# Optimization experiments

Hardware: AMD Instinct MI355X
Metric: run time of the kernel (lower is better)

The kernel has to match this reference:

```python
import jax, jax.numpy as jnp
import numpy as np

N = 10000      # nodes
E = 320000     # edges
H = 128        # hidden_features
GF = 12        # graph-level features
L = 6          # gnn layers
EPS = 1e-5


def _glorot(key, shape):
    fan_in = shape[0]
    return (jax.random.normal(key, shape, jnp.float32) / np.sqrt(fan_in)).astype(jnp.float32)


def periodic_difference(x_i, x_j, domain):
    diff = x_i - x_j
    # (1 - 2*(x_i < x_j)) * domain  ==  +domain if x_i >= x_j else -domain
    shift = jnp.where(x_i < x_j, -domain, domain)
    diff_shifted = diff - shift
    return jnp.where(jnp.abs(diff) < jnp.abs(diff_shifted), diff, diff_shifted)


def _mlp2_relu(x, W1, b1, W2, b2):
    # Linear -> ReLU -> Linear -> ReLU
    return jax.nn.relu(jax.nn.relu(x @ W1 + b1) @ W2 + b2)


def setup_inputs() -> dict:
    key = jax.random.key(0)
    ks = jax.random.split(key, 32)
    inp = {
        "v": jax.random.normal(ks[0], (N, 6), jnp.float32),
        "pos": jax.random.uniform(ks[1], (N, 3), jnp.float32),
        "r": jax.random.uniform(ks[2], (N, 1), jnp.float32),
        "domain": jnp.ones((3,), jnp.float32),
        "t": jax.random.uniform(ks[3], (1,), jnp.float32),
        "x_global": jax.random.normal(ks[4], (4,), jnp.float32),
        "domain_next": jnp.ones((3,), jnp.float32),
        "t_next": jax.random.uniform(ks[5], (1,), jnp.float32),
        "edge_index": jax.random.randint(ks[6], (2, E), 0, N, jnp.int32),
        "batch": jnp.zeros((N,), jnp.int32),
    }
    # embedding MLP: 19 -> H -> H
    inp["emb_W1"] = _glorot(ks[7], (19, H)); inp["emb_b1"] = jnp.zeros((H,), jnp.float32)
    inp["emb_W2"] = _glorot(ks[8], (H, H)); inp["emb_b2"] = jnp.zeros((H,), jnp.float32)
    # per-layer message net: 157 -> H -> H ; update net: 268 -> H -> H
    msg_in = H + GF + 3 + 2 * (6 + 1)   # 157
    upd_in = H + H + GF                 # 268
    inp["msg_W1"] = jnp.stack([_glorot(jax.random.fold_in(ks[9], i), (msg_in, H)) for i in range(L)])
    inp["msg_b1"] = jnp.zeros((L, H), jnp.float32)
    inp["msg_W2"] = jnp.stack([_glorot(jax.random.fold_in(ks[10], i), (H, H)) for i in range(L)])
    inp["msg_b2"] = jnp.zeros((L, H), jnp.float32)
    inp["upd_W1"] = jnp.stack([_glorot(jax.random.fold_in(ks[11], i), (upd_in, H)) for i in range(L)])
    inp["upd_b1"] = jnp.zeros((L, H), jnp.float32)
    inp["upd_W2"] = jnp.stack([_glorot(jax.random.fold_in(ks[12], i), (H, H)) for i in range(L)])
    inp["upd_b2"] = jnp.zeros((L, H), jnp.float32)
    # output MLP: H -> H -> 9 ; macro MLP: H -> H -> 3
    inp["out_W1"] = _glorot(ks[13], (H, H)); inp["out_b1"] = jnp.zeros((H,), jnp.float32)
    inp["out_W2"] = _glorot(ks[14], (H, 9)); inp["out_b2"] = jnp.zeros((9,), jnp.float32)
    inp["mac_W1"] = _glorot(ks[15], (H, H)); inp["mac_b1"] = jnp.zeros((H,), jnp.float32)
    inp["mac_W2"] = _glorot(ks[16], (H, 3)); inp["mac_b2"] = jnp.zeros((3,), jnp.float32)
    return inp


def reference(v, pos, r, domain, t, x_global, domain_next, t_next, edge_index, batch,
              emb_W1, emb_b1, emb_W2, emb_b2,
              msg_W1, msg_b1, msg_W2, msg_b2,
              upd_W1, upd_b1, upd_W2, upd_b2,
              out_W1, out_b1, out_W2, out_b2,
              mac_W1, mac_b1, mac_W2, mac_b2):
    n = v.shape[0]
    gf = jnp.concatenate([domain, t, x_global, domain_next, t_next])          # [12]
    gf_n = jnp.broadcast_to(gf, (n, GF))
    node_features = jnp.concatenate([pos, v], axis=1)                         # [N, 9]

    # embedding (positions excluded)
    h = _mlp2_relu(jnp.concatenate([r, v, gf_n], axis=1), emb_W1, emb_b1, emb_W2, emb_b2)

    src, dst = edge_index[0], edge_index[1]   # j = source, i = target (PyG default)
    gf_e = jnp.broadcast_to(gf, (src.shape[0], GF))
    counts = jax.ops.segment_sum(jnp.ones(src.shape, h.dtype), dst, num_segments=N)
    inv_counts = (1.0 / jnp.maximum(counts, 1.0))[:, None]

    pos_diff = periodic_difference(pos[dst], pos[src], domain)                # [E, 3]
    v_i, v_j, r_i, r_j = v[dst], v[src], r[dst], r[src]

    for l in range(L):
        h_i, h_j = h[dst], h[src]
        msg_in = jnp.concatenate([h_i - h_j, v_i, v_j, r_i, r_j, pos_diff, gf_e], axis=1)
        m = _mlp2_relu(msg_in, msg_W1[l], msg_b1[l], msg_W2[l], msg_b2[l])    # [E, H]
        agg = jax.ops.segment_sum(m, dst, num_segments=N) * inv_counts        # scatter-mean
        upd_in = jnp.concatenate([h, agg, gf_n], axis=1)
        u = _mlp2_relu(upd_in, upd_W1[l], upd_b1[l], upd_W2[l], upd_b2[l])
        h = u + h                                                              # residual (in==out)
        # InstanceNorm over each graph (single graph here), biased variance
        mu = h.mean(axis=0, keepdims=True)
        var = h.var(axis=0, keepdims=True)
        h = (h - mu) / jnp.sqrt(var + EPS)

    prediction = jax.nn.relu(h @ out_W1 + out_b1) @ out_W2 + out_b2 + node_features
    pred_x = jnp.remainder(prediction[:, :3], domain_next)
    pred_v = prediction[:, 3:]
    h_mean = h.mean(axis=0)                                                    # global mean pool, 1 graph
    pred_macro = jax.nn.relu(h_mean @ mac_W1 + mac_b1) @ mac_W2 + mac_b2
    return pred_x, pred_v, pred_macro
```

## Files before the change

### kernel.cpp

```cpp
#include <hip/hip_runtime.h>
#include <hip/hip_bf16.h>

#define NN 10000
#define NE 320000
#define HD 128
#define NL 6
#define EPSV 1e-5f

typedef _Float16 half8  __attribute__((ext_vector_type(8)));
typedef _Float16 half4v __attribute__((ext_vector_type(4)));
typedef float    f32x4  __attribute__((ext_vector_type(4)));

__device__ __forceinline__ float relu_(float x){ return fmaxf(x, 0.0f); }


__global__ void k_degree(const int* __restrict__ dst, int* __restrict__ counts){
  int e = blockIdx.x*256 + threadIdx.x;
  if (e < NE) atomicAdd(&counts[dst[e]], 1);
}

__global__ void k_scan(const int* __restrict__ counts, int* __restrict__ offs, float* __restrict__ invc){
  __shared__ int lds[1024];
  __shared__ int base_s;
  int tid = threadIdx.x;
  if (tid==0) base_s = 0;
  __syncthreads();
  for (int start=0; start<NN; start+=1024){
    int i = start+tid;
    int vv = (i<NN)? counts[i] : 0;
    lds[tid]=vv; __syncthreads();
    for (int off=1; off<1024; off<<=1){
      int t = (tid>=off)? lds[tid-off] : 0;
      __syncthreads();
      lds[tid] += t;
      __syncthreads();
    }
    int incl = lds[tid];
    if (i<NN){
      offs[i] = base_s + incl - vv;
      invc[i] = 1.0f / fmaxf((float)vv, 1.0f);
    }
    __syncthreads();
    if (tid==1023) base_s += lds[1023];
    __syncthreads();
  }
  if (tid==0) offs[NN] = base_s;
}

__global__ void k_place(const int* __restrict__ src, const int* __restrict__ dst,
                        const int* __restrict__ offs, int* __restrict__ cursor, int* __restrict__ csr){
  int e = blockIdx.x*256 + threadIdx.x;
  if (e < NE){
    int d = dst[e];
    int p = atomicAdd(&cursor[d], 1);
    csr[offs[d]+p] = src[e];
  }
}


__global__ void k_biasfold(const float* __restrict__ dom, const float* __restrict__ tt,
                           const float* __restrict__ xg, const float* __restrict__ domn,
                           const float* __restrict__ tn,
                           const float* __restrict__ embW1, const float* __restrict__ embB1,
                           const float* __restrict__ msgW1, const float* __restrict__ msgB1,
                           const float* __restrict__ updW1, const float* __restrict__ updB1,
                           float* __restrict__ b1eff, float* __restrict__ mu, float* __restrict__ rstd){
  float gf[12];
  gf[0]=dom[0]; gf[1]=dom[1]; gf[2]=dom[2]; gf[3]=tt[0];
  gf[4]=xg[0]; gf[5]=xg[1]; gf[6]=xg[2]; gf[7]=xg[3];
  gf[8]=domn[0]; gf[9]=domn[1]; gf[10]=domn[2]; gf[11]=tn[0];
  int b = blockIdx.x, t = threadIdx.x;
  if (b==0){
    float s = embB1[t];
    #pragma unroll
    for (int k=0;k<12;++k) s += gf[k]*embW1[(7+k)*HD + t];
    b1eff[t] = s;
  } else if (b<=6){
    int l=b-1;
    float s = msgB1[l*HD+t];
    #pragma unroll
    for (int k=0;k<12;++k) s += gf[k]*msgW1[((size_t)l*157 + 145+k)*HD + t];
    b1eff[(1+l)*HD + t] = s;
  } else if (b<=12){
    int l=b-7;
    float s = updB1[l*HD+t];
    #pragma unroll
    for (int k=0;k<12;++k) s += gf[k]*updW1[((size_t)l*268 + 256+k)*HD + t];
    b1eff[(7+l)*HD + t] = s;
  } else {
    mu[t] = 0.f;
    rstd[t] = 1.f;
  }
}


__global__ __launch_bounds__(512,1) void k_embed(
    const float* __restrict__ r, const float* __restrict__ v,
    const float* __restrict__ W1, const float* __restrict__ b1e,
    const float* __restrict__ W2, const float* __restrict__ b2,
    float* __restrict__ hb){
  __shared__ alignas(16) _Float16 Ahi[16*136];
  __shared__ alignas(16) _Float16 Alo[16*136];
  int tid = threadIdx.x;
  int n0 = blockIdx.x*16;
  if (tid < 256){
    int node = tid>>4, chunk = tid&15;
    int n = n0 + node;
    int f = chunk*8;
    float in7[7];
    in7[0]=r[n];
    #pragma unroll
    for (int k=0;k<6;++k) in7[1+k]=v[n*6+k];
    half8 ah, al;
    #pragma unroll
    for (int j=0;j<8;++j){
      float z = b1e[f+j];
      #pragma unroll
      for (int k=0;k<7;++k) z += in7[k]*W1[k*HD + f+j];
      float a = fmaxf(z, 0.f);
      _Float16 h = (_Float16)a;
      ah[j] = h; al[j] = (_Float16)(a - (float)h);
    }
    *(half8*)&Ahi[node*136 + f] = ah;
    *(half8*)&Alo[node*136 + f] = al;
  }
  int wid = tid>>6, lane = tid&63, g = lane>>4, c = lane&15;
  int col = 16*wid + c;
  half8 bh[4], bl[4];
  #pragma unroll
  for (int ks=0; ks<4; ++ks){
    half8 fh, fl;
    #pragma unroll
    for (int j=0;j<8;++j){
      float w = W2[(size_t)(ks*32 + g*8 + j)*HD + col];
      _Float16 h = (_Float16)w;
      fh[j]=h; fl[j]=(_Float16)(w - (float)h);
    }
    bh[ks]=fh; bl[ks]=fl;
  }
  float b2c = b2[col];
  f32x4 zero4 = {0.f,0.f,0.f,0.f};
  __syncthreads();
  f32x4 d = zero4;
  #pragma unroll
  for (int ks=0; ks<4; ++ks){
    half8 ah = *(const half8*)&Ahi[c*136 + ks*32 + g*8];
    half8 al = *(const half8*)&Alo[c*136 + ks*32 + g*8];
    d = __builtin_amdgcn_mfma_f32_16x16x32_f16(ah, bh[ks], d, 0,0,0);
    d = __builtin_amdgcn_mfma_f32_16x16x32_f16(al, bh[ks], d, 0,0,0);
    d = __builtin_amdgcn_mfma_f32_16x16x32_f16(ah, bl[ks], d, 0,0,0);
  }
  #pragma unroll
  for (int jj=0;jj<4;++jj){
    int n = n0 + g*4 + jj;
    hb[(size_t)n*HD + col] = fmaxf(d[jj] + b2c, 0.f);
  }
}


__global__ __launch_bounds__(512,1) void k_hW(
    const float* __restrict__ hb, const float* __restrict__ mu, const float* __restrict__ rstd,
    const float* __restrict__ v, const float* __restrict__ r,
    const float* __restrict__ W, const float* __restrict__ b1e,
    float* __restrict__ P, float* __restrict__ Q){
  __shared__ alignas(16) _Float16 Xhi[16*136];
  __shared__ alignas(16) _Float16 Xlo[16*136];
  int tid = threadIdx.x;
  int n0 = blockIdx.x*16;
  if (tid < 256){
    int node = tid>>4, chunk = tid&15;
    int n = n0 + node;
    int f = chunk*8;
    half8 xh, xl;
    #pragma unroll
    for (int j=0;j<8;++j){
      float x = (hb[(size_t)n*HD + f+j] - mu[f+j]) * rstd[f+j];
      _Float16 h = (_Float16)x;
      xh[j] = h; xl[j] = (_Float16)(x - (float)h);
    }
    *(half8*)&Xhi[node*136 + f] = xh;
    *(half8*)&Xlo[node*136 + f] = xl;
  }
  int wid = tid>>6, lane = tid&63, g = lane>>4, c = lane&15;
  int col = 16*wid + c;
  half8 bh[4], bl[4];
  #pragma unroll
  for (int ks=0; ks<4; ++ks){
    half8 fh, fl;
    #pragma unroll
    for (int j=0;j<8;++j){
      float w = W[(size_t)(ks*32 + g*8 + j)*HD + col];
      _Float16 h = (_Float16)w;
      fh[j]=h; fl[j]=(_Float16)(w - (float)h);
    }
    bh[ks]=fh; bl[ks]=fl;
  }
  float wvi[6], wvj[6];
  #pragma unroll
  for (int x=0;x<6;++x){
    wvi[x]=W[(size_t)(128+x)*HD+col];
    wvj[x]=W[(size_t)(134+x)*HD+col];
  }
  float wri=W[(size_t)140*HD+col], wrj=W[(size_t)141*HD+col];
  float b1c=b1e[col];
  f32x4 zero4 = {0.f,0.f,0.f,0.f};
  __syncthreads();
  f32x4 d = zero4;
  #pragma unroll
  for (int ks=0; ks<4; ++ks){
    half8 ah = *(const half8*)&Xhi[c*136 + ks*32 + g*8];
    half8 al = *(const half8*)&Xlo[c*136 + ks*32 + g*8];
    d = __builtin_amdgcn_mfma_f32_16x16x32_f16(ah, bh[ks], d, 0,0,0);
    d = __builtin_amdgcn_mfma_f32_16x16x32_f16(al, bh[ks], d, 0,0,0);
    d = __builtin_amdgcn_mfma_f32_16x16x32_f16(ah, bl[ks], d, 0,0,0);
  }
  #pragma unroll
  for (int jj=0;jj<4;++jj){
    int n = n0 + g*4 + jj;
    float m = d[jj];
    float p = m + b1c, q = -m;
    #pragma unroll
    for (int x=0;x<6;++x){
      float vx = v[n*6+x];
      p += vx*wvi[x]; q += vx*wvj[x];
    }
    float rn = r[n];
    p += rn*wri; q += rn*wrj;
    P[(size_t)n*HD+col]=p;
    Q[(size_t)n*HD+col]=q;
  }
}


__global__ __launch_bounds__(256,2) void k_edge(
    const float* __restrict__ P, const float* __restrict__ Q,
    const float* __restrict__ pos, const float* __restrict__ dom,
    const int* __restrict__ offs, const int* __restrict__ csr,
    const float* __restrict__ Wpd, const float* __restrict__ W2, const float* __restrict__ b2,
    const float* __restrict__ invc, float* __restrict__ agg,
    float* __restrict__ zsum, float* __restrict__ zsumsq){
  __shared__ alignas(16) _Float16 w1pd[128*40];
  __shared__ alignas(16) _Float16 a1hi[16*136];
  __shared__ alignas(16) _Float16 a1lo[16*136];
  int tid = threadIdx.x;
  if (blockIdx.x==0 && tid<HD){ zsum[tid]=0.f; zsumsq[tid]=0.f; }
  if (tid < 128){
    int f = tid;
    #pragma unroll
    for (int k=0;k<32;++k) w1pd[f*40+k] = (_Float16)0.f;
    #pragma unroll
    for (int x=0;x<3;++x){
      float w = Wpd[x*HD + f];
      _Float16 h = (_Float16)w;
      w1pd[f*40 + x]     = h;
      w1pd[f*40 + 3 + x] = h;
      w1pd[f*40 + 6 + x] = (_Float16)(w - (float)h);
    }
  }
  int wid = tid>>6, lane = tid&63, g = lane>>4, c = lane&15;
  int t0 = 2*wid, t1 = 2*wid+1;
  half8 w2h[4][2], w2l[4][2];
  #pragma unroll
  for (int ks=0; ks<4; ++ks){
    #pragma unroll
    for (int tt=0; tt<2; ++tt){
      int col = 16*(2*wid+tt) + c;
      half8 fh, fl;
      #pragma unroll
      for (int j=0;j<8;++j){
        float w = W2[(ks*32 + g*8 + j)*HD + col];
        _Float16 h = (_Float16)w;
        fh[j] = h;
        fl[j] = (_Float16)(w - (float)h);
      }
      w2h[ks][tt] = fh;
      w2l[ks][tt] = fl;
    }
  }
  float b2v0 = b2[16*t0 + c], b2v1 = b2[16*t1 + c];
  float dm0=dom[0], dm1=dom[1], dm2=dom[2];
  f32x4 zero4 = {0.f,0.f,0.f,0.f};
  __syncthreads();
  int n0 = blockIdx.x*2;
  for (int n = n0; n < n0+2; ++n){
    f32x4 pv0 = *(const f32x4*)(P + (size_t)n*HD + 16*t0 + 4*g);
    f32x4 pv1 = *(const f32x4*)(P + (size_t)n*HD + 16*t1 + 4*g);
    float pn0=pos[n*3+0], pn1=pos[n*3+1], pn2=pos[n*3+2];
    float acc0=0.f, acc1=0.f;
    int ib=offs[n], ie=offs[n+1];
    for (int base=ib; base<ie; base+=16){
      int nb = ie - base; if (nb>16) nb = 16;
      int sA = csr[base + ((c<nb)? c : nb-1)];
      float q0=pos[sA*3+0], q1=pos[sA*3+1], q2=pos[sA*3+2];
      float pd0,pd1,pd2;
      { float diff,sh,ds;
        diff=pn0-q0; sh=(pn0<q0)?-dm0:dm0; ds=diff-sh; pd0=(fabsf(diff)<fabsf(ds))?diff:ds;
        diff=pn1-q1; sh=(pn1<q1)?-dm1:dm1; ds=diff-sh; pd1=(fabsf(diff)<fabsf(ds))?diff:ds;
        diff=pn2-q2; sh=(pn2<q2)?-dm2:dm2; ds=diff-sh; pd2=(fabsf(diff)<fabsf(ds))?diff:ds;
      }
      _Float16 p0h = (_Float16)pd0, p1h = (_Float16)pd1, p2h = (_Float16)pd2;
      _Float16 p0l = (_Float16)(pd0 - (float)p0h);
      _Float16 p1l = (_Float16)(pd1 - (float)p1h);
      _Float16 p2l = (_Float16)(pd2 - (float)p2h);
      half8 pdf;
      #pragma unroll
      for (int j=0;j<8;++j) pdf[j]=(_Float16)0.f;
      if (g==0){ pdf[0]=p0h; pdf[1]=p1h; pdf[2]=p2h; pdf[3]=p0l; pdf[4]=p1l; pdf[5]=p2l; pdf[6]=p0h; pdf[7]=p1h; }
      else if (g==1){ pdf[0]=p2h; }
      half8 w1f0 = *(const half8*)&w1pd[(16*t0 + c)*40 + g*8];
      half8 w1f1 = *(const half8*)&w1pd[(16*t1 + c)*40 + g*8];
      f32x4 d0 = __builtin_amdgcn_mfma_f32_16x16x32_f16(w1f0, pdf, zero4, 0,0,0);
      f32x4 d1 = __builtin_amdgcn_mfma_f32_16x16x32_f16(w1f1, pdf, zero4, 0,0,0);
      const float* Qs = Q + (size_t)sA*HD;
      f32x4 qv0 = *(const f32x4*)(Qs + 16*t0 + 4*g);
      f32x4 qv1 = *(const f32x4*)(Qs + 16*t1 + 4*g);
      half4v h0, l0, h1, l1;
      #pragma unroll
      for (int j=0;j<4;++j){
        float a = fmaxf(d0[j] + pv0[j] + qv0[j], 0.f);
        _Float16 hh = (_Float16)a;
        h0[j] = hh; l0[j] = (_Float16)(a - (float)hh);
        float b = fmaxf(d1[j] + pv1[j] + qv1[j], 0.f);
        _Float16 hb2 = (_Float16)b;
        h1[j] = hb2; l1[j] = (_Float16)(b - (float)hb2);
      }
      *(half4v*)&a1hi[c*136 + 16*t0 + 4*g] = h0;
      *(half4v*)&a1lo[c*136 + 16*t0 + 4*g] = l0;
      *(half4v*)&a1hi[c*136 + 16*t1 + 4*g] = h1;
      *(half4v*)&a1lo[c*136 + 16*t1 + 4*g] = l1;
      __syncthreads();
      f32x4 m0 = zero4, m1 = zero4;
      #pragma unroll
      for (int ks=0; ks<4; ++ks){
        half8 ah = *(const half8*)&a1hi[c*136 + ks*32 + g*8];
        half8 al = *(const half8*)&a1lo[c*136 + ks*32 + g*8];
        m0 = __builtin_amdgcn_mfma_f32_16x16x32_f16(ah, w2h[ks][0], m0, 0,0,0);
        m0 = __builtin_amdgcn_mfma_f32_16x16x32_f16(al, w2h[ks][0], m0, 0,0,0);
        m0 = __builtin_amdgcn_mfma_f32_16x16x32_f16(ah, w2l[ks][0], m0, 0,0,0);
        m1 = __builtin_amdgcn_mfma_f32_16x16x32_f16(ah, w2h[ks][1], m1, 0,0,0);
        m1 = __builtin_amdgcn_mfma_f32_16x16x32_f16(al, w2h[ks][1], m1, 0,0,0);
        m1 = __builtin_amdgcn_mfma_f32_16x16x32_f16(ah, w2l[ks][1], m1, 0,0,0);
      }
      if (nb == 16){
        acc0 += fmaxf(m0[0]+b2v0,0.f)+fmaxf(m0[1]+b2v0,0.f)+fmaxf(m0[2]+b2v0,0.f)+fmaxf(m0[3]+b2v0,0.f);
        acc1 += fmaxf(m1[0]+b2v1,0.f)+fmaxf(m1[1]+b2v1,0.f)+fmaxf(m1[2]+b2v1,0.f)+fmaxf(m1[3]+b2v1,0.f);
      } else {
        #pragma unroll
        for (int j=0;j<4;++j){
          if (4*g+j < nb){
            acc0 += fmaxf(m0[j]+b2v0, 0.f);
            acc1 += fmaxf(m1[j]+b2v1, 0.f);
          }
        }
      }
      __syncthreads();
    }
    acc0 += __shfl_xor(acc0, 16); acc0 += __shfl_xor(acc0, 32);
    acc1 += __shfl_xor(acc1, 16); acc1 += __shfl_xor(acc1, 32);
    if (g==0){
      float ic = invc[n];
      agg[n*HD + 16*t0 + c] = acc0*ic;
      agg[n*HD + 16*t1 + c] = acc1*ic;
    }
  }
}


__global__ __launch_bounds__(512,1) void k_upd(
    float* __restrict__ hb, const float* __restrict__ mu, const float* __restrict__ rstd,
    const float* __restrict__ agg,
    const float* __restrict__ U1, const float* __restrict__ b1e,
    const float* __restrict__ U2, const float* __restrict__ bs2,
    float* __restrict__ sum, float* __restrict__ sumsq){
  __shared__ alignas(16) _Float16 Xhi[16*264];
  __shared__ alignas(16) _Float16 Xlo[16*264];
  __shared__ alignas(16) _Float16 Ahi[16*136];
  __shared__ alignas(16) _Float16 Alo[16*136];
  int tid = threadIdx.x;
  int n0 = blockIdx.x*16;
  {
    int node = tid>>5, chunk = tid&31;
    int n = n0 + node;
    int f = chunk*8;
    half8 xh, xl;
    if (f < 128){
      #pragma unroll
      for (int j=0;j<8;++j){
        float x = (hb[(size_t)n*HD + f+j] - mu[f+j]) * rstd[f+j];
        _Float16 h = (_Float16)x;
        xh[j] = h; xl[j] = (_Float16)(x - (float)h);
      }
    } else {
      #pragma unroll
      for (int j=0;j<8;++j){
        float x = agg[(size_t)n*HD + (f-128)+j];
        _Float16 h = (_Float16)x;
        xh[j] = h; xl[j] = (_Float16)(x - (float)h);
      }
    }
    *(half8*)&Xhi[node*264 + f] = xh;
    *(half8*)&Xlo[node*264 + f] = xl;
  }
  int wid = tid>>6, lane = tid&63, g = lane>>4, c = lane&15;
  int col = 16*wid + c;
  half8 b1h[8], b1l[8], b2h[4], b2l[4];
  #pragma unroll
  for (int ks=0; ks<8; ++ks){
    half8 fh, fl;
    #pragma unroll
    for (int j=0;j<8;++j){
      float w = U1[(size_t)(ks*32 + g*8 + j)*HD + col];
      _Float16 h = (_Float16)w;
      fh[j]=h; fl[j]=(_Float16)(w - (float)h);
    }
    b1h[ks]=fh; b1l[ks]=fl;
  }
  #pragma unroll
  for (int ks=0; ks<4; ++ks){
    half8 fh, fl;
    #pragma unroll
    for (int j=0;j<8;++j){
      float w = U2[(size_t)(ks*32 + g*8 + j)*HD + col];
      _Float16 h = (_Float16)w;
      fh[j]=h; fl[j]=(_Float16)(w - (float)h);
    }
    b2h[ks]=fh; b2l[ks]=fl;
  }
  f32x4 zero4 = {0.f,0.f,0.f,0.f};
  __syncthreads();
  f32x4 d = zero4;
  #pragma unroll
  for (int ks=0; ks<8; ++ks){
    half8 ah = *(const half8*)&Xhi[c*264 + ks*32 + g*8];
    half8 al = *(const half8*)&Xlo[c*264 + ks*32 + g*8];
    d = __builtin_amdgcn_mfma_f32_16x16x32_f16(ah, b1h[ks], d, 0,0,0);
    d = __builtin_amdgcn_mfma_f32_16x16x32_f16(al, b1h[ks], d, 0,0,0);
    d = __builtin_amdgcn_mfma_f32_16x16x32_f16(ah, b1l[ks], d, 0,0,0);
  }
  {
    float bb = b1e[col];
    #pragma unroll
    for (int jj=0;jj<4;++jj){
      float a = fmaxf(d[jj] + bb, 0.f);
      _Float16 h = (_Float16)a;
      Ahi[(g*4+jj)*136 + col] = h;
      Alo[(g*4+jj)*136 + col] = (_Float16)(a - (float)h);
    }
  }
  __syncthreads();
  f32x4 u = zero4;
  #pragma unroll
  for (int ks=0; ks<4; ++ks){
    half8 ah = *(const half8*)&Ahi[c*136 + ks*32 + g*8];
    half8 al = *(const half8*)&Alo[c*136 + ks*32 + g*8];
    u = __builtin_amdgcn_mfma_f32_16x16x32_f16(ah, b2h[ks], u, 0,0,0);
    u = __builtin_amdgcn_mfma_f32_16x16x32_f16(al, b2h[ks], u, 0,0,0);
    u = __builtin_amdgcn_mfma_f32_16x16x32_f16(ah, b2l[ks], u, 0,0,0);
  }
  float bc = bs2[col];
  float mc = mu[col], rc = rstd[col];
  float s=0.f, q=0.f;
  #pragma unroll
  for (int jj=0;jj<4;++jj){
    int n = n0 + g*4 + jj;
    float hn = (hb[(size_t)n*HD + col] - mc)*rc;
    float b0 = hn + fmaxf(u[jj] + bc, 0.f);
    hb[(size_t)n*HD + col] = b0;
    s += b0; q += b0*b0;
  }
  s += __shfl_xor(s,16); s += __shfl_xor(s,32);
  q += __shfl_xor(q,16); q += __shfl_xor(q,32);
  if (g==0){
    atomicAdd(&sum[col], s);
    atomicAdd(&sumsq[col], q);
  }
}

__global__ void k_normfin(const float* __restrict__ sum, const float* __restrict__ sumsq,
                          float* __restrict__ mu, float* __restrict__ rstd){
  int t=threadIdx.x;
  float m = sum[t]*(1.0f/NN);
  float var = sumsq[t]*(1.0f/NN) - m*m;
  mu[t]=m;
  rstd[t]=rsqrtf(fmaxf(var,0.0f)+EPSV);
}


__global__ void k_out(const float* __restrict__ hb, const float* __restrict__ mu, const float* __restrict__ rstd,
                      const float* __restrict__ pos, const float* __restrict__ v,
                      const float* __restrict__ W1, const float* __restrict__ b1,
                      const float* __restrict__ W2, const float* __restrict__ b2,
                      const float* __restrict__ domn, float* __restrict__ out){
  __shared__ alignas(16) float hs[4][HD*4];
  __shared__ alignas(16) float a1s[4][HD*4];
  int tid=threadIdx.x, wid=tid>>6, lane=tid&63;
  int gw=blockIdx.x*4+wid;
  int f0=lane, f1=lane+64;
  float* h4=hs[wid];
  float* a1p=a1s[wid];
  int n0=gw*4;
  float mu0=mu[f0], mu1=mu[f1], rs0=rstd[f0], rs1=rstd[f1];
  float4 hv0,hv1;
  hv0.x=(hb[(n0+0)*HD+f0]-mu0)*rs0; hv0.y=(hb[(n0+1)*HD+f0]-mu0)*rs0;
  hv0.z=(hb[(n0+2)*HD+f0]-mu0)*rs0; hv0.w=(hb[(n0+3)*HD+f0]-mu0)*rs0;
  hv1.x=(hb[(n0+0)*HD+f1]-mu1)*rs1; hv1.y=(hb[(n0+1)*HD+f1]-mu1)*rs1;
  hv1.z=(hb[(n0+2)*HD+f1]-mu1)*rs1; hv1.w=(hb[(n0+3)*HD+f1]-mu1)*rs1;
  *(float4*)&h4[f0*4]=hv0; *(float4*)&h4[f1*4]=hv1;
  float b1f0=b1[f0], b1f1=b1[f1];
  float zf0[4]={b1f0,b1f0,b1f0,b1f0}, zf1[4]={b1f1,b1f1,b1f1,b1f1};
  for (int k=0;k<HD;++k){
    float4 a = *(const float4*)&h4[k*4];
    float w0=W1[k*HD+f0], w1=W1[k*HD+f1];
    zf0[0]+=a.x*w0; zf1[0]+=a.x*w1;
    zf0[1]+=a.y*w0; zf1[1]+=a.y*w1;
    zf0[2]+=a.z*w0; zf1[2]+=a.z*w1;
    zf0[3]+=a.w*w0; zf1[3]+=a.w*w1;
  }
  *(float4*)&a1p[f0*4] = make_float4(relu_(zf0[0]),relu_(zf0[1]),relu_(zf0[2]),relu_(zf0[3]));
  *(float4*)&a1p[f1*4] = make_float4(relu_(zf1[0]),relu_(zf1[1]),relu_(zf1[2]),relu_(zf1[3]));
  if (lane < 36){
    int e = lane/9, j = lane - e*9;
    int n = n0+e;
    float p = b2[j];
    for (int k=0;k<HD;++k) p += a1p[k*4+e]*W2[k*9+j];
    if (j<3){
      p += pos[n*3+j];
      float d = domn[j];
      p = p - floorf(p/d)*d;
      out[n*3+j] = p;
    } else {
      p += v[n*6 + (j-3)];
      out[3*NN + n*6 + (j-3)] = p;
    }
  }
}

__global__ void k_macro(const float* __restrict__ sum, const float* __restrict__ mu, const float* __restrict__ rstd,
                        const float* __restrict__ W1, const float* __restrict__ b1,
                        const float* __restrict__ W2, const float* __restrict__ b2,
                        float* __restrict__ out){
  __shared__ float hm[HD];
  __shared__ float as[HD];
  int t=threadIdx.x;
  hm[t] = (sum[t]*(1.0f/NN) - mu[t])*rstd[t];
  __syncthreads();
  float z=b1[t];
  for (int k=0;k<HD;++k) z += hm[k]*W1[k*HD+t];
  as[t]=relu_(z);
  __syncthreads();
  if (t<3){
    float p=b2[t];
    for (int k=0;k<HD;++k) p += as[k]*W2[k*3+t];
    out[9*NN+t]=p;
  }
}


extern "C" void kernel_launch(void* const* d_in, const int* in_sizes, int n_in,
                              void* d_out, int out_size, void* d_ws, size_t ws_size,
                              hipStream_t stream) {
  const float* v    = (const float*)d_in[0];
  const float* pos  = (const float*)d_in[1];
  const float* r    = (const float*)d_in[2];
  const float* dom  = (const float*)d_in[3];
  const float* tt   = (const float*)d_in[4];
  const float* xg   = (const float*)d_in[5];
  const float* domn = (const float*)d_in[6];
  const float* tn   = (const float*)d_in[7];
  const int*   eidx = (const int*)d_in[8];
  const float* embW1 = (const float*)d_in[10];
  const float* embB1 = (const float*)d_in[11];
  const float* embW2 = (const float*)d_in[12];
  const float* embB2 = (const float*)d_in[13];
  const float* msgW1 = (const float*)d_in[14];
  const float* msgB1 = (const float*)d_in[15];
  const float* msgW2 = (const float*)d_in[16];
  const float* msgB2 = (const float*)d_in[17];
  const float* updW1 = (const float*)d_in[18];
  const float* updB1 = (const float*)d_in[19];
  const float* updW2 = (const float*)d_in[20];
  const float* updB2 = (const float*)d_in[21];
  const float* outW1 = (const float*)d_in[22];
  const float* outB1 = (const float*)d_in[23];
  const float* outW2 = (const float*)d_in[24];
  const float* outB2 = (const float*)d_in[25];
  const float* macW1 = (const float*)d_in[26];
  const float* macB1 = (const float*)d_in[27];
  const float* macW2 = (const float*)d_in[28];
  const float* macB2 = (const float*)d_in[29];
  float* out = (float*)d_out;
  float* ws  = (float*)d_ws;

  float* hb    = ws;
  float* P     = ws + 1280000;
  float* Q     = ws + 2560000;
  float* agg   = ws + 3840000;
  float* invc  = ws + 5120000;
  float* b1eff = ws + 5130000;
  float* sum   = ws + 5131664;
  float* sumsq = ws + 5131792;
  float* mu    = ws + 5131920;
  float* rstd  = ws + 5132048;
  int* counts  = (int*)(ws + 5132304);
  int* offs    = counts + NN;
  int* cursor  = offs + NN + 1;
  int* csr     = cursor + NN;

  const int* srcA = eidx;
  const int* dstA = eidx + NE;

  hipMemsetAsync(counts, 0, NN*sizeof(int), stream);
  hipMemsetAsync(cursor, 0, NN*sizeof(int), stream);

  k_degree<<<(NE+255)/256, 256, 0, stream>>>(dstA, counts);
  k_scan<<<1, 1024, 0, stream>>>(counts, offs, invc);
  k_place<<<(NE+255)/256, 256, 0, stream>>>(srcA, dstA, offs, cursor, csr);
  k_biasfold<<<14, 128, 0, stream>>>(dom, tt, xg, domn, tn, embW1, embB1, msgW1, msgB1, updW1, updB1,
                                     b1eff, mu, rstd);
  k_embed<<<625, 512, 0, stream>>>(r, v, embW1, b1eff, embW2, embB2, hb);

  for (int l=0; l<NL; ++l){
    k_hW<<<625,512,0,stream>>>(hb, mu, rstd, v, r, msgW1 + (size_t)l*157*HD, b1eff + (1+l)*HD, P, Q);
    k_edge<<<5000,256,0,stream>>>(P, Q, pos, dom, offs, csr,
        msgW1 + ((size_t)l*157+142)*HD,
        msgW2 + (size_t)l*HD*HD, msgB2 + l*HD, invc, agg, sum, sumsq);
    k_upd<<<625,512,0,stream>>>(hb, mu, rstd, agg,
        updW1 + (size_t)l*268*HD, b1eff + (7+l)*HD,
        updW2 + (size_t)l*HD*HD, updB2 + l*HD, sum, sumsq);
    k_normfin<<<1,128,0,stream>>>(sum, sumsq, mu, rstd);
  }

  k_out<<<625,256,0,stream>>>(hb, mu, rstd, pos, v, outW1, outB1, outW2, outB2, domn, out);
  k_macro<<<1,128,0,stream>>>(sum, mu, rstd, macW1, macB1, macW2, macB2, out);
}
```

Before: 840.7 us.

## Process 32 edges per sync in edge kernel and move output MLP to MFMA

The edge kernel now processes two 16-edge sub-tiles per iteration, so it issues one pair of barriers per 32 edges instead of per 16. The per-edge W1 position-feature fragment loads are hoisted out of the loop into registers. The output head kernel is rewritten to use split-fp16 MFMA for both layers on 16-node tiles with 512 threads, replacing the scalar FMA loop. The larger LDS tiles and extra registers may reduce occupancy, and low-degree nodes waste more of the larger tile.

Measured after the change: 930.1 us. 10.6% more time.

```diff
diff --git a/kernel.cpp b/kernel.cpp
--- a/kernel.cpp
+++ b/kernel.cpp
@@ -240,8 +240,8 @@
     const float* __restrict__ invc, float* __restrict__ agg,
     float* __restrict__ zsum, float* __restrict__ zsumsq){
   __shared__ alignas(16) _Float16 w1pd[128*40];
-  __shared__ alignas(16) _Float16 a1hi[16*136];
-  __shared__ alignas(16) _Float16 a1lo[16*136];
+  __shared__ alignas(16) _Float16 a1hi[32*136];
+  __shared__ alignas(16) _Float16 a1lo[32*136];
   int tid = threadIdx.x;
   if (blockIdx.x==0 && tid<HD){ zsum[tid]=0.f; zsumsq[tid]=0.f; }
   if (tid < 128){
@@ -280,7 +280,10 @@
   float b2v0 = b2[16*t0 + c], b2v1 = b2[16*t1 + c];
   float dm0=dom[0], dm1=dom[1], dm2=dom[2];
   f32x4 zero4 = {0.f,0.f,0.f,0.f};
-  __syncthreads();
+  half8 w1f0 = *(const half8*)&w1pd[(16*t0 + c)*40 + g*8];
+  __syncthreads();
+  w1f0 = *(const half8*)&w1pd[(16*t0 + c)*40 + g*8];
+  half8 w1f1 = *(const half8*)&w1pd[(16*t1 + c)*40 + g*8];
   int n0 = blockIdx.x*2;
   for (int n = n0; n < n0+2; ++n){
     f32x4 pv0 = *(const f32x4*)(P + (size_t)n*HD + 16*t0 + 4*g);
@@ -288,68 +291,106 @@
     float pn0=pos[n*3+0], pn1=pos[n*3+1], pn2=pos[n*3+2];
     float acc0=0.f, acc1=0.f;
     int ib=offs[n], ie=offs[n+1];
-    for (int base=ib; base<ie; base+=16){
-      int nb = ie - base; if (nb>16) nb = 16;
-      int sA = csr[base + ((c<nb)? c : nb-1)];
-      float q0=pos[sA*3+0], q1=pos[sA*3+1], q2=pos[sA*3+2];
-      float pd0,pd1,pd2;
-      { float diff,sh,ds;
-        diff=pn0-q0; sh=(pn0<q0)?-dm0:dm0; ds=diff-sh; pd0=(fabsf(diff)<fabsf(ds))?diff:ds;
-        diff=pn1-q1; sh=(pn1<q1)?-dm1:dm1; ds=diff-sh; pd1=(fabsf(diff)<fabsf(ds))?diff:ds;
-        diff=pn2-q2; sh=(pn2<q2)?-dm2:dm2; ds=diff-sh; pd2=(fabsf(diff)<fabsf(ds))?diff:ds;
-      }
-      _Float16 p0h = (_Float16)pd0, p1h = (_Float16)pd1, p2h = (_Float16)pd2;
-      _Float16 p0l = (_Float16)(pd0 - (float)p0h);
-      _Float16 p1l = (_Float16)(pd1 - (float)p1h);
-      _Float16 p2l = (_Float16)(pd2 - (float)p2h);
-      half8 pdf;
-      #pragma unroll
-      for (int j=0;j<8;++j) pdf[j]=(_Float16)0.f;
-      if (g==0){ pdf[0]=p0h; pdf[1]=p1h; pdf[2]=p2h; pdf[3]=p0l; pdf[4]=p1l; pdf[5]=p2l; pdf[6]=p0h; pdf[7]=p1h; }
-      else if (g==1){ pdf[0]=p2h; }
-      half8 w1f0 = *(const half8*)&w1pd[(16*t0 + c)*40 + g*8];
-      half8 w1f1 = *(const half8*)&w1pd[(16*t1 + c)*40 + g*8];
-      f32x4 d0 = __builtin_amdgcn_mfma_f32_16x16x32_f16(w1f0, pdf, zero4, 0,0,0);
-      f32x4 d1 = __builtin_amdgcn_mfma_f32_16x16x32_f16(w1f1, pdf, zero4, 0,0,0);
-      const float* Qs = Q + (size_t)sA*HD;
-      f32x4 qv0 = *(const f32x4*)(Qs + 16*t0 + 4*g);
-      f32x4 qv1 = *(const f32x4*)(Qs + 16*t1 + 4*g);
-      half4v h0, l0, h1, l1;
-      #pragma unroll
-      for (int j=0;j<4;++j){
-        float a = fmaxf(d0[j] + pv0[j] + qv0[j], 0.f);
-        _Float16 hh = (_Float16)a;
-        h0[j] = hh; l0[j] = (_Float16)(a - (float)hh);
-        float b = fmaxf(d1[j] + pv1[j] + qv1[j], 0.f);
-        _Float16 hb2 = (_Float16)b;
-        h1[j] = hb2; l1[j] = (_Float16)(b - (float)hb2);
-      }
-      *(half4v*)&a1hi[c*136 + 16*t0 + 4*g] = h0;
-      *(half4v*)&a1lo[c*136 + 16*t0 + 4*g] = l0;
-      *(half4v*)&a1hi[c*136 + 16*t1 + 4*g] = h1;
-      *(half4v*)&a1lo[c*136 + 16*t1 + 4*g] = l1;
-      __syncthreads();
-      f32x4 m0 = zero4, m1 = zero4;
-      #pragma unroll
-      for (int ks=0; ks<4; ++ks){
-        half8 ah = *(const half8*)&a1hi[c*136 + ks*32 + g*8];
-        half8 al = *(const half8*)&a1lo[c*136 + ks*32 + g*8];
-        m0 = __builtin_amdgcn_mfma_f32_16x16x32_f16(ah, w2h[ks][0], m0, 0,0,0);
-        m0 = __builtin_amdgcn_mfma_f32_16x16x32_f16(al, w2h[ks][0], m0, 0,0,0);
-        m0 = __builtin_amdgcn_mfma_f32_16x16x32_f16(ah, w2l[ks][0], m0, 0,0,0);
-        m1 = __builtin_amdgcn_mfma_f32_16x16x32_f16(ah, w2h[ks][1], m1, 0,0,0);
-        m1 = __builtin_amdgcn_mfma_f32_16x16x32_f16(al, w2h[ks][1], m1, 0,0,0);
-        m1 = __builtin_amdgcn_mfma_f32_16x16x32_f16(ah, w2l[ks][1], m1, 0,0,0);
-      }
-      if (nb == 16){
-        acc0 += fmaxf(m0[0]+b2v0,0.f)+fmaxf(m0[1]+b2v0,0.f)+fmaxf(m0[2]+b2v0,0.f)+fmaxf(m0[3]+b2v0,0.f);
-        acc1 += fmaxf(m1[0]+b2v1,0.f)+fmaxf(m1[1]+b2v1,0.f)+fmaxf(m1[2]+b2v1,0.f)+fmaxf(m1[3]+b2v1,0.f);
-      } else {
+    for (int base=ib; base<ie; base+=32){
+      int nb = ie - base; if (nb>32) nb = 32;
+      {
+        int sA = csr[base + ((c<nb)? c : nb-1)];
+        float q0=pos[sA*3+0], q1=pos[sA*3+1], q2=pos[sA*3+2];
+        float pd0,pd1,pd2;
+        { float diff,sh,ds;
+          diff=pn0-q0; sh=(pn0<q0)?-dm0:dm0; ds=diff-sh; pd0=(fabsf(diff)<fabsf(ds))?diff:ds;
+          diff=pn1-q1; sh=(pn1<q1)?-dm1:dm1; ds=diff-sh; pd1=(fabsf(diff)<fabsf(ds))?diff:ds;
+          diff=pn2-q2; sh=(pn2<q2)?-dm2:dm2; ds=diff-sh; pd2=(fabsf(diff)<fabsf(ds))?diff:ds;
+        }
+        _Float16 p0h=(_Float16)pd0, p1h=(_Float16)pd1, p2h=(_Float16)pd2;
+        _Float16 p0l=(_Float16)(pd0-(float)p0h), p1l=(_Float16)(pd1-(float)p1h), p2l=(_Float16)(pd2-(float)p2h);
+        half8 pdf;
+        #pragma unroll
+        for (int j=0;j<8;++j) pdf[j]=(_Float16)0.f;
+        if (g==0){ pdf[0]=p0h; pdf[1]=p1h; pdf[2]=p2h; pdf[3]=p0l; pdf[4]=p1l; pdf[5]=p2l; pdf[6]=p0h; pdf[7]=p1h; }
+        else if (g==1){ pdf[0]=p2h; }
+        f32x4 d0 = __builtin_amdgcn_mfma_f32_16x16x32_f16(w1f0, pdf, zero4, 0,0,0);
+        f32x4 d1 = __builtin_amdgcn_mfma_f32_16x16x32_f16(w1f1, pdf, zero4, 0,0,0);
+        const float* Qs = Q + (size_t)sA*HD;
+        f32x4 qv0 = *(const f32x4*)(Qs + 16*t0 + 4*g);
+        f32x4 qv1 = *(const f32x4*)(Qs + 16*t1 + 4*g);
+        half4v h0, l0, h1, l1;
         #pragma unroll
         for (int j=0;j<4;++j){
-          if (4*g+j < nb){
-            acc0 += fmaxf(m0[j]+b2v0, 0.f);
-            acc1 += fmaxf(m1[j]+b2v1, 0.f);
+          float a = fmaxf(d0[j] + pv0[j] + qv0[j], 0.f);
+          _Float16 hh = (_Float16)a;
+          h0[j] = hh; l0[j] = (_Float16)(a - (float)hh);
+          float b = fmaxf(d1[j] + pv1[j] + qv1[j], 0.f);
+          _Float16 hb2 = (_Float16)b;
+          h1[j] = hb2; l1[j] = (_Float16)(b - (float)hb2);
+        }
+        *(half4v*)&a1hi[c*136 + 16*t0 + 4*g] = h0;
+        *(half4v*)&a1lo[c*136 + 16*t0 + 4*g] = l0;
+        *(half4v*)&a1hi[c*136 + 16*t1 + 4*g] = h1;
+        *(half4v*)&a1lo[c*136 + 16*t1 + 4*g] = l1;
+      }
+      {
+        int sA = csr[base + ((16+c<nb)? 16+c : nb-1)];
+        float q0=pos[sA*3+0], q1=pos[sA*3+1], q2=pos[sA*3+2];
+        float pd0,pd1,pd2;
+        { float diff,sh,ds;
+          diff=pn0-q0; sh=(pn0<q0)?-dm0:dm0; ds=diff-sh; pd0=(fabsf(diff)<fabsf(ds))?diff:ds;
+          diff=pn1-q1; sh=(pn1<q1)?-dm1:dm1; ds=diff-sh; pd1=(fabsf(diff)<fabsf(ds))?diff:ds;
+          diff=pn2-q2; sh=(pn2<q2)?-dm2:dm2; ds=diff-sh; pd2=(fabsf(diff)<fabsf(ds))?diff:ds;
+        }
+        _Float16 p0h=(_Float16)pd0, p1h=(_Float16)pd1, p2h=(_Float16)pd2;
+        _Float16 p0l=(_Float16)(pd0-(float)p0h), p1l=(_Float16)(pd1-(float)p1h), p2l=(_Float16)(pd2-(float)p2h);
+        half8 pdf;
+        #pragma unroll
+        for (int j=0;j<8;++j) pdf[j]=(_Float16)0.f;
+        if (g==0){ pdf[0]=p0h; pdf[1]=p1h; pdf[2]=p2h; pdf[3]=p0l; pdf[4]=p1l; pdf[5]=p2l; pdf[6]=p0h; pdf[7]=p1h; }
+        else if (g==1){ pdf[0]=p2h; }
+        f32x4 d0 = __builtin_amdgcn_mfma_f32_16x16x32_f16(w1f0, pdf, zero4, 0,0,0);
+        f32x4 d1 = __builtin_amdgcn_mfma_f32_16x16x32_f16(w1f1, pdf, zero4, 0,0,0);
+        const float* Qs = Q + (size_t)sA*HD;
+        f32x4 qv0 = *(const f32x4*)(Qs + 16*t0 + 4*g);
+        f32x4 qv1 = *(const f32x4*)(Qs + 16*t1 + 4*g);
+        half4v h0, l0, h1, l1;
+        #pragma unroll
+        for (int j=0;j<4;++j){
+          float a = fmaxf(d0[j] + pv0[j] + qv0[j], 0.f);
+          _Float16 hh = (_Float16)a;
+          h0[j] = hh; l0[j] = (_Float16)(a - (float)hh);
+          float b = fmaxf(d1[j] + pv1[j] + qv1[j], 0.f);
+          _Float16 hb2 = (_Float16)b;
+          h1[j] = hb2; l1[j] = (_Float16)(b - (float)hb2);
+        }
+        *(half4v*)&a1hi[(16+c)*136 + 16*t0 + 4*g] = h0;
+        *(half4v*)&a1lo[(16+c)*136 + 16*t0 + 4*g] = l0;
+        *(half4v*)&a1hi[(16+c)*136 + 16*t1 + 4*g] = h1;
+        *(half4v*)&a1lo[(16+c)*136 + 16*t1 + 4*g] = l1;
+      }
+      __syncthreads();
+      #pragma unroll
+      for (int R=0; R<2; ++R){
+        f32x4 m0 = zero4, m1 = zero4;
+        #pragma unroll
+        for (int ks=0; ks<4; ++ks){
+          half8 ah = *(const half8*)&a1hi[(R*16+c)*136 + ks*32 + g*8];
+          half8 al = *(const half8*)&a1lo[(R*16+c)*136 + ks*32 + g*8];
+          m0 = __builtin_amdgcn_mfma_f32_16x16x32_f16(ah, w2h[ks][0], m0, 0,0,0);
+          m0 = __builtin_amdgcn_mfma_f32_16x16x32_f16(al, w2h[ks][0], m0, 0,0,0);
+          m0 = __builtin_amdgcn_mfma_f32_16x16x32_f16(ah, w2l[ks][0], m0, 0,0,0);
+          m1 = __builtin_amdgcn_mfma_f32_16x16x32_f16(ah, w2h[ks][1], m1, 0,0,0);
+          m1 = __builtin_amdgcn_mfma_f32_16x16x32_f16(al, w2h[ks][1], m1, 0,0,0);
+          m1 = __builtin_amdgcn_mfma_f32_16x16x32_f16(ah, w2l[ks][1], m1, 0,0,0);
+        }
+        int e0 = R*16 + 4*g;
+        if (nb >= e0+4){
+          acc0 += fmaxf(m0[0]+b2v0,0.f)+fmaxf(m0[1]+b2v0,0.f)+fmaxf(m0[2]+b2v0,0.f)+fmaxf(m0[3]+b2v0,0.f);
+          acc1 += fmaxf(m1[0]+b2v1,0.f)+fmaxf(m1[1]+b2v1,0.f)+fmaxf(m1[2]+b2v1,0.f)+fmaxf(m1[3]+b2v1,0.f);
+        } else {
+          #pragma unroll
+          for (int j=0;j<4;++j){
+            if (e0+j < nb){
+              acc0 += fmaxf(m0[j]+b2v0, 0.f);
+              acc1 += fmaxf(m1[j]+b2v1, 0.f);
+            }
           }
         }
       }
@@ -486,51 +527,106 @@
 }
 
 
-__global__ void k_out(const float* __restrict__ hb, const float* __restrict__ mu, const float* __restrict__ rstd,
-                      const float* __restrict__ pos, const float* __restrict__ v,
-                      const float* __restrict__ W1, const float* __restrict__ b1,
-                      const float* __restrict__ W2, const float* __restrict__ b2,
-                      const float* __restrict__ domn, float* __restrict__ out){
-  __shared__ alignas(16) float hs[4][HD*4];
-  __shared__ alignas(16) float a1s[4][HD*4];
-  int tid=threadIdx.x, wid=tid>>6, lane=tid&63;
-  int gw=blockIdx.x*4+wid;
-  int f0=lane, f1=lane+64;
-  float* h4=hs[wid];
-  float* a1p=a1s[wid];
-  int n0=gw*4;
-  float mu0=mu[f0], mu1=mu[f1], rs0=rstd[f0], rs1=rstd[f1];
-  float4 hv0,hv1;
-  hv0.x=(hb[(n0+0)*HD+f0]-mu0)*rs0; hv0.y=(hb[(n0+1)*HD+f0]-mu0)*rs0;
-  hv0.z=(hb[(n0+2)*HD+f0]-mu0)*rs0; hv0.w=(hb[(n0+3)*HD+f0]-mu0)*rs0;
-  hv1.x=(hb[(n0+0)*HD+f1]-mu1)*rs1; hv1.y=(hb[(n0+1)*HD+f1]-mu1)*rs1;
-  hv1.z=(hb[(n0+2)*HD+f1]-mu1)*rs1; hv1.w=(hb[(n0+3)*HD+f1]-mu1)*rs1;
-  *(float4*)&h4[f0*4]=hv0; *(float4*)&h4[f1*4]=hv1;
-  float b1f0=b1[f0], b1f1=b1[f1];
-  float zf0[4]={b1f0,b1f0,b1f0,b1f0}, zf1[4]={b1f1,b1f1,b1f1,b1f1};
-  for (int k=0;k<HD;++k){
-    float4 a = *(const float4*)&h4[k*4];
-    float w0=W1[k*HD+f0], w1=W1[k*HD+f1];
-    zf0[0]+=a.x*w0; zf1[0]+=a.x*w1;
-    zf0[1]+=a.y*w0; zf1[1]+=a.y*w1;
-    zf0[2]+=a.z*w0; zf1[2]+=a.z*w1;
-    zf0[3]+=a.w*w0; zf1[3]+=a.w*w1;
-  }
-  *(float4*)&a1p[f0*4] = make_float4(relu_(zf0[0]),relu_(zf0[1]),relu_(zf0[2]),relu_(zf0[3]));
-  *(float4*)&a1p[f1*4] = make_float4(relu_(zf1[0]),relu_(zf1[1]),relu_(zf1[2]),relu_(zf1[3]));
-  if (lane < 36){
-    int e = lane/9, j = lane - e*9;
-    int n = n0+e;
-    float p = b2[j];
-    for (int k=0;k<HD;++k) p += a1p[k*4+e]*W2[k*9+j];
-    if (j<3){
-      p += pos[n*3+j];
-      float d = domn[j];
-      p = p - floorf(p/d)*d;
-      out[n*3+j] = p;
-    } else {
-      p += v[n*6 + (j-3)];
-      out[3*NN + n*6 + (j-3)] = p;
+__global__ __launch_bounds__(512,1) void k_out(
+    const float* __restrict__ hb, const float* __restrict__ mu, const float* __restrict__ rstd,
+    const float* __restrict__ pos, const float* __restrict__ v,
+    const float* __restrict__ W1, const float* __restrict__ b1,
+    const float* __restrict__ W2, const float* __restrict__ b2,
+    const float* __restrict__ domn, float* __restrict__ out){
+  __shared__ alignas(16) _Float16 Xhi[16*136];
+  __shared__ alignas(16) _Float16 Xlo[16*136];
+  __shared__ alignas(16) _Float16 Ahi[16*136];
+  __shared__ alignas(16) _Float16 Alo[16*136];
+  int tid = threadIdx.x;
+  int n0 = blockIdx.x*16;
+  if (tid < 256){
+    int node = tid>>4, chunk = tid&15;
+    int n = n0 + node;
+    int f = chunk*8;
+    half8 xh, xl;
+    #pragma unroll
+    for (int j=0;j<8;++j){
+      float x = (hb[(size_t)n*HD + f+j] - mu[f+j]) * rstd[f+j];
+      _Float16 h = (_Float16)x;
+      xh[j] = h; xl[j] = (_Float16)(x - (float)h);
+    }
+    *(half8*)&Xhi[node*136 + f] = xh;
+    *(half8*)&Xlo[node*136 + f] = xl;
+  }
+  int wid = tid>>6, lane = tid&63, g = lane>>4, c = lane&15;
+  int col = 16*wid + c;
+  half8 bh[4], bl[4];
+  #pragma unroll
+  for (int ks=0; ks<4; ++ks){
+    half8 fh, fl;
+    #pragma unroll
+    for (int j=0;j<8;++j){
+      float w = W1[(size_t)(ks*32 + g*8 + j)*HD + col];
+      _Float16 h = (_Float16)w;
+      fh[j]=h; fl[j]=(_Float16)(w - (float)h);
+    }
+    bh[ks]=fh; bl[ks]=fl;
+  }
+  half8 w9h[4], w9l[4];
+  if (wid==0){
+    #pragma unroll
+    for (int ks=0; ks<4; ++ks){
+      half8 fh, fl;
+      #pragma unroll
+      for (int j=0;j<8;++j){
+        float w = (c<9)? W2[(size_t)(ks*32 + g*8 + j)*9 + c] : 0.f;
+        _Float16 h = (_Float16)w;
+        fh[j]=h; fl[j]=(_Float16)(w - (float)h);
+      }
+      w9h[ks]=fh; w9l[ks]=fl;
+    }
+  }
+  float b1c = b1[col];
+  f32x4 zero4 = {0.f,0.f,0.f,0.f};
+  __syncthreads();
+  f32x4 d = zero4;
+  #pragma unroll
+  for (int ks=0; ks<4; ++ks){
+    half8 ah = *(const half8*)&Xhi[c*136 + ks*32 + g*8];
+    half8 al = *(const half8*)&Xlo[c*136 + ks*32 + g*8];
+    d = __builtin_amdgcn_mfma_f32_16x16x32_f16(ah, bh[ks], d, 0,0,0);
+    d = __builtin_amdgcn_mfma_f32_16x16x32_f16(al, bh[ks], d, 0,0,0);
+    d = __builtin_amdgcn_mfma_f32_16x16x32_f16(ah, bl[ks], d, 0,0,0);
+  }
+  #pragma unroll
+  for (int jj=0;jj<4;++jj){
+    float a = fmaxf(d[jj] + b1c, 0.f);
+    _Float16 h = (_Float16)a;
+    Ahi[(g*4+jj)*136 + col] = h;
+    Alo[(g*4+jj)*136 + col] = (_Float16)(a - (float)h);
+  }
+  __syncthreads();
+  if (wid==0){
+    f32x4 u = zero4;
+    #pragma unroll
+    for (int ks=0; ks<4; ++ks){
+      half8 ah = *(const half8*)&Ahi[c*136 + ks*32 + g*8];
+      half8 al = *(const half8*)&Alo[c*136 + ks*32 + g*8];
+      u = __builtin_amdgcn_mfma_f32_16x16x32_f16(ah, w9h[ks], u, 0,0,0);
+      u = __builtin_amdgcn_mfma_f32_16x16x32_f16(al, w9h[ks], u, 0,0,0);
+      u = __builtin_amdgcn_mfma_f32_16x16x32_f16(ah, w9l[ks], u, 0,0,0);
+    }
+    if (c < 9){
+      float bc = b2[c];
+      #pragma unroll
+      for (int jj=0;jj<4;++jj){
+        int n = n0 + g*4 + jj;
+        float p = u[jj] + bc;
+        if (c < 3){
+          p += pos[n*3+c];
+          float dd = domn[c];
+          p = p - floorf(p/dd)*dd;
+          out[n*3+c] = p;
+        } else {
+          p += v[n*6 + (c-3)];
+          out[3*NN + n*6 + (c-3)] = p;
+        }
+      }
     }
   }
 }
@@ -630,6 +726,6 @@
     k_normfin<<<1,128,0,stream>>>(sum, sumsq, mu, rstd);
   }
 
-  k_out<<<625,256,0,stream>>>(hb, mu, rstd, pos, v, outW1, outB1, outW2, outB2, domn, out);
+  k_out<<<625,512,0,stream>>>(hb, mu, rstd, pos, v, outW1, outB1, outW2, outB2, domn, out);
   k_macro<<<1,128,0,stream>>>(sum, mu, rstd, macW1, macB1, macW2, macB2, out);
 }
```
